# Performance work log

Measured on AMD Instinct MI355X. Metric: run time of the kernel, lower is better.

The kernel has to match this reference:

```python
import jax, jax.numpy as jnp
import numpy as np

B, N, IN_DIM, OUT_DIM, K = 64, 256, 512, 512, 8
DK = OUT_DIM // K  # per-kernel feature dim


def setup_inputs() -> dict:
    key = jax.random.key(0)
    k1, k2, k3, k4 = jax.random.split(key, 4)
    node_feats = jax.random.normal(k1, (B, N, IN_DIM), dtype=jnp.float32)
    adj = jax.random.uniform(k2, (B, K, N, N), dtype=jnp.float32)
    weight = jax.random.normal(k3, (IN_DIM, OUT_DIM), dtype=jnp.float32) * (1.0 / np.sqrt(IN_DIM))
    bias = jax.random.normal(k4, (OUT_DIM,), dtype=jnp.float32) * 0.01
    return {"node_feats": node_feats, "adj": adj, "weight": weight, "bias": bias}


def reference(node_feats, adj, weight, bias):
    # kernel linear + ReLU: (b, n, out_dim)
    h = jax.nn.relu(jnp.einsum('bni,io->bno', node_feats, weight) + bias)
    # split into kernel slots: (b, n, k, dk)
    h = h.reshape(B, N, K, DK)
    # graph.aggregate: per-kernel dense message passing over adjacency
    # out[b,n,k,d] = sum_m adj[b,k,n,m] * h[b,m,k,d]
    agg = jnp.einsum('bknm,bmkd->bnkd', adj, h)
    return agg.reshape(B, N, OUT_DIM)
```

## Files before the change

kernel.cpp:

```cpp
#include <hip/hip_runtime.h>
#include <hip/hip_bf16.h>


typedef __attribute__((ext_vector_type(8))) short short8;
typedef __attribute__((ext_vector_type(4))) float floatx4;

__device__ __forceinline__ unsigned short f2bf(float f) {
    union { float f; unsigned u; } v; v.f = f;
    unsigned r = v.u + 0x7FFFu + ((v.u >> 16) & 1u);
    return (unsigned short)(r >> 16);
}

__device__ __forceinline__ unsigned pk2bf(float a, float b) {
    union { __hip_bfloat162 h; unsigned u; } cv;
    cv.h = __float22bfloat162_rn(make_float2(a, b));
    return cv.u;
}

__global__ __launch_bounds__(256) void wt_kernel(const float* __restrict__ W,
                                                 unsigned short* __restrict__ Wt) {
    __shared__ unsigned short t_lds[64 * 66];
    const int tile = blockIdx.x;
    const int k0 = (tile >> 3) * 64;
    const int o0 = (tile & 7) * 64;
    const int t = threadIdx.x;
    const int c = t & 63;
    const int rb = t >> 6;
#pragma unroll
    for (int i = 0; i < 16; ++i) {
        int r = i * 4 + rb;
        t_lds[c * 66 + r] = f2bf(W[(size_t)(k0 + r) * 512 + o0 + c]);
    }
    __syncthreads();
#pragma unroll
    for (int i = 0; i < 16; ++i) {
        int o_r = i * 4 + rb;
        Wt[(size_t)(o0 + o_r) * 512 + k0 + c] = t_lds[o_r * 66 + c];
    }
}

__global__ __launch_bounds__(1024, 8) void fused_kernel(
    const float* __restrict__ X, const unsigned short* __restrict__ Wt,
    const float* __restrict__ bias, const float* __restrict__ adj,
    float* __restrict__ out) {
    __shared__ unsigned short ht[64 * 256];

    const int id = blockIdx.x;
    const int b = id & 63;
    const int ks = id >> 6;

    const int tid = threadIdx.x;
    const int lane = tid & 63, w = tid >> 6;
    const int lrow = lane & 15, quad = lane >> 4;

    const float* Xb = X + (size_t)b * 256 * 512;
    const unsigned short* Wslice = Wt + (size_t)ks * 64 * 512;

    floatx4 acc1[4];
    const floatx4 fzero = {0.f, 0.f, 0.f, 0.f};
#pragma unroll
    for (int j = 0; j < 4; ++j) acc1[j] = fzero;

    const float* xrow = Xb + (size_t)(w * 16 + lrow) * 512 + quad * 8;
    const unsigned short* wrow = Wslice + (size_t)lrow * 512 + quad * 8;

#pragma unroll 2
    for (int kb = 0; kb < 16; ++kb) {
        const int k0 = kb * 32;
        float4 xa = *(const float4*)(xrow + k0);
        float4 xc = *(const float4*)(xrow + k0 + 4);
        union { short8 s; unsigned u[4]; } af;
        af.u[0] = pk2bf(xa.x, xa.y);
        af.u[1] = pk2bf(xa.z, xa.w);
        af.u[2] = pk2bf(xc.x, xc.y);
        af.u[3] = pk2bf(xc.z, xc.w);
#pragma unroll
        for (int j = 0; j < 4; ++j) {
            short8 bfr = *(const short8*)(wrow + (size_t)j * 16 * 512 + k0);
            acc1[j] = __builtin_amdgcn_mfma_f32_16x16x32_bf16(af.s, bfr, acc1[j], 0, 0, 0);
        }
    }

#pragma unroll
    for (int j = 0; j < 4; ++j) {
        int d = 16 * j + lrow;
        float bv = bias[ks * 64 + d];
        floatx4 c = acc1[j];
        unsigned p01 = pk2bf(fmaxf(c.x + bv, 0.f), fmaxf(c.y + bv, 0.f));
        unsigned p23 = pk2bf(fmaxf(c.z + bv, 0.f), fmaxf(c.w + bv, 0.f));
        int jm = 2 * w + (quad >> 1);
        int phys = jm ^ (d & 7);
        unsigned* d32 = (unsigned*)(ht + d * 256 + phys * 8 + (quad & 1) * 4);
        d32[0] = p01; d32[1] = p23;
    }
    __syncthreads();

    const float* Abase = adj + ((size_t)(b * 8 + ks)) * 65536;
    const float* arow = Abase + (size_t)(w * 16 + lrow) * 256 + quad * 8;

    floatx4 acc[4];
#pragma unroll
    for (int j = 0; j < 4; ++j) acc[j] = fzero;

#pragma unroll 2
    for (int mt = 0; mt < 8; ++mt) {
        float4 a0 = *(const float4*)(arow + mt * 32);
        float4 a1 = *(const float4*)(arow + mt * 32 + 4);
        union { short8 s; unsigned u[4]; } afr;
        afr.u[0] = pk2bf(a0.x, a0.y);
        afr.u[1] = pk2bf(a0.z, a0.w);
        afr.u[2] = pk2bf(a1.x, a1.y);
        afr.u[3] = pk2bf(a1.z, a1.w);
        const int jm = 4 * mt + quad;
#pragma unroll
        for (int dt = 0; dt < 4; ++dt) {
            int d = dt * 16 + lrow;
            short8 bfr = *(const short8*)(ht + d * 256 + ((jm ^ (d & 7)) * 8));
            acc[dt] = __builtin_amdgcn_mfma_f32_16x16x32_bf16(afr.s, bfr, acc[dt], 0, 0, 0);
        }
    }

    const int n_g = w * 16 + quad * 4;
    float* dst = out + ((size_t)b * 256 + n_g) * 512 + ks * 64 + lrow;
#pragma unroll
    for (int dt = 0; dt < 4; ++dt) {
        float* p = dst + dt * 16;
        p[0 * 512] = acc[dt].x;
        p[1 * 512] = acc[dt].y;
        p[2 * 512] = acc[dt].z;
        p[3 * 512] = acc[dt].w;
    }
}

extern "C" void kernel_launch(void* const* d_in, const int* in_sizes, int n_in,
                              void* d_out, int out_size, void* d_ws, size_t ws_size,
                              hipStream_t stream) {
    const float* X    = (const float*)d_in[0];
    const float* adj  = (const float*)d_in[1];
    const float* W    = (const float*)d_in[2];
    const float* bias = (const float*)d_in[3];
    float* out = (float*)d_out;

    unsigned short* Wt = (unsigned short*)d_ws;

    wt_kernel<<<64, 256, 0, stream>>>(W, Wt);
    fused_kernel<<<512, 1024, 0, stream>>>(X, Wt, bias, adj, out);
}
```

Baseline: 305.6 us.

## Halve block size, give each wave two row tiles, and double-buffer global loads

The fused kernel now runs 512 threads per block instead of 1024, with each wave handling 32 rows (two 16-row tiles) in both GEMM stages. Each W/ht fragment load is then shared across two MFMA row groups. Both loops are fully unrolled and prefetch the next step's X/W and adj values into registers while the current step computes, and the first-stage adj load is issued before the LDS write. The goal is to hide global load latency and cut redundant B-fragment loads, at the cost of higher register pressure and fewer waves in flight per block.

```diff
diff --git a/kernel.cpp b/kernel.cpp
--- a/kernel.cpp
+++ b/kernel.cpp
@@ -39,7 +39,7 @@
     }
 }
 
-__global__ __launch_bounds__(1024, 8) void fused_kernel(
+__global__ __launch_bounds__(512, 4) void fused_kernel(
     const float* __restrict__ X, const unsigned short* __restrict__ Wt,
     const float* __restrict__ bias, const float* __restrict__ adj,
     float* __restrict__ out) {
@@ -52,83 +52,137 @@
     const int tid = threadIdx.x;
     const int lane = tid & 63, w = tid >> 6;
     const int lrow = lane & 15, quad = lane >> 4;
+    const int m0 = w * 32;
 
     const float* Xb = X + (size_t)b * 256 * 512;
     const unsigned short* Wslice = Wt + (size_t)ks * 64 * 512;
 
-    floatx4 acc1[4];
+    const float* xrow0 = Xb + (size_t)(m0 + lrow) * 512 + quad * 8;
+    const float* xrow1 = xrow0 + 16 * 512;
+    const unsigned short* wrow = Wslice + (size_t)lrow * 512 + quad * 8;
+
+    float bv[4];
+#pragma unroll
+    for (int j = 0; j < 4; ++j) bv[j] = bias[ks * 64 + 16 * j + lrow];
+
+    floatx4 acc1[2][4];
     const floatx4 fzero = {0.f, 0.f, 0.f, 0.f};
 #pragma unroll
-    for (int j = 0; j < 4; ++j) acc1[j] = fzero;
-
-    const float* xrow = Xb + (size_t)(w * 16 + lrow) * 512 + quad * 8;
-    const unsigned short* wrow = Wslice + (size_t)lrow * 512 + quad * 8;
-
-#pragma unroll 2
+    for (int g = 0; g < 2; ++g)
+#pragma unroll
+        for (int j = 0; j < 4; ++j) acc1[g][j] = fzero;
+
+    float4 xb_[2][2][2];
+    short8 wb_[2][4];
+
+#define LOAD_S1(buf, kb) do {                                           \
+        const int k0_ = (kb) * 32;                                      \
+        xb_[buf][0][0] = *(const float4*)(xrow0 + k0_);                 \
+        xb_[buf][0][1] = *(const float4*)(xrow0 + k0_ + 4);             \
+        xb_[buf][1][0] = *(const float4*)(xrow1 + k0_);                 \
+        xb_[buf][1][1] = *(const float4*)(xrow1 + k0_ + 4);             \
+        wb_[buf][0] = *(const short8*)(wrow + k0_);                     \
+        wb_[buf][1] = *(const short8*)(wrow + 16 * 512 + k0_);          \
+        wb_[buf][2] = *(const short8*)(wrow + 32 * 512 + k0_);          \
+        wb_[buf][3] = *(const short8*)(wrow + 48 * 512 + k0_);          \
+    } while (0)
+
+    LOAD_S1(0, 0);
+#pragma unroll
     for (int kb = 0; kb < 16; ++kb) {
-        const int k0 = kb * 32;
-        float4 xa = *(const float4*)(xrow + k0);
-        float4 xc = *(const float4*)(xrow + k0 + 4);
-        union { short8 s; unsigned u[4]; } af;
-        af.u[0] = pk2bf(xa.x, xa.y);
-        af.u[1] = pk2bf(xa.z, xa.w);
-        af.u[2] = pk2bf(xc.x, xc.y);
-        af.u[3] = pk2bf(xc.z, xc.w);
+        const int cur = kb & 1;
+        if (kb < 15) LOAD_S1(cur ^ 1, kb + 1);
+#pragma unroll
+        for (int g = 0; g < 2; ++g) {
+            union { short8 s; unsigned u[4]; } af;
+            const float4 va = xb_[cur][g][0], vc = xb_[cur][g][1];
+            af.u[0] = pk2bf(va.x, va.y);
+            af.u[1] = pk2bf(va.z, va.w);
+            af.u[2] = pk2bf(vc.x, vc.y);
+            af.u[3] = pk2bf(vc.z, vc.w);
+#pragma unroll
+            for (int j = 0; j < 4; ++j)
+                acc1[g][j] = __builtin_amdgcn_mfma_f32_16x16x32_bf16(
+                    af.s, wb_[cur][j], acc1[g][j], 0, 0, 0);
+        }
+    }
+#undef LOAD_S1
+
+    const float* Abase = adj + ((size_t)(b * 8 + ks)) * 65536;
+    const float* arow0 = Abase + (size_t)(m0 + lrow) * 256 + quad * 8;
+    const float* arow1 = arow0 + 16 * 256;
+
+    float4 ab_[2][2][2];
+#define LOAD_S2(buf, mt) do {                                           \
+        ab_[buf][0][0] = *(const float4*)(arow0 + (mt) * 32);           \
+        ab_[buf][0][1] = *(const float4*)(arow0 + (mt) * 32 + 4);       \
+        ab_[buf][1][0] = *(const float4*)(arow1 + (mt) * 32);           \
+        ab_[buf][1][1] = *(const float4*)(arow1 + (mt) * 32 + 4);       \
+    } while (0)
+
+    LOAD_S2(0, 0);
+
+#pragma unroll
+    for (int g = 0; g < 2; ++g) {
 #pragma unroll
         for (int j = 0; j < 4; ++j) {
-            short8 bfr = *(const short8*)(wrow + (size_t)j * 16 * 512 + k0);
-            acc1[j] = __builtin_amdgcn_mfma_f32_16x16x32_bf16(af.s, bfr, acc1[j], 0, 0, 0);
-        }
-    }
-
-#pragma unroll
-    for (int j = 0; j < 4; ++j) {
-        int d = 16 * j + lrow;
-        float bv = bias[ks * 64 + d];
-        floatx4 c = acc1[j];
-        unsigned p01 = pk2bf(fmaxf(c.x + bv, 0.f), fmaxf(c.y + bv, 0.f));
-        unsigned p23 = pk2bf(fmaxf(c.z + bv, 0.f), fmaxf(c.w + bv, 0.f));
-        int jm = 2 * w + (quad >> 1);
-        int phys = jm ^ (d & 7);
-        unsigned* d32 = (unsigned*)(ht + d * 256 + phys * 8 + (quad & 1) * 4);
-        d32[0] = p01; d32[1] = p23;
+            int d = 16 * j + lrow;
+            floatx4 c = acc1[g][j];
+            unsigned p01 = pk2bf(fmaxf(c.x + bv[j], 0.f), fmaxf(c.y + bv[j], 0.f));
+            unsigned p23 = pk2bf(fmaxf(c.z + bv[j], 0.f), fmaxf(c.w + bv[j], 0.f));
+            int jm = 4 * w + 2 * g + (quad >> 1);
+            int phys = jm ^ (d & 7);
+            unsigned* d32 = (unsigned*)(ht + d * 256 + phys * 8 + (quad & 1) * 4);
+            d32[0] = p01; d32[1] = p23;
+        }
     }
     __syncthreads();
 
-    const float* Abase = adj + ((size_t)(b * 8 + ks)) * 65536;
-    const float* arow = Abase + (size_t)(w * 16 + lrow) * 256 + quad * 8;
-
-    floatx4 acc[4];
-#pragma unroll
-    for (int j = 0; j < 4; ++j) acc[j] = fzero;
-
-#pragma unroll 2
+    floatx4 acc2[2][4];
+#pragma unroll
+    for (int g = 0; g < 2; ++g)
+#pragma unroll
+        for (int j = 0; j < 4; ++j) acc2[g][j] = fzero;
+
+#pragma unroll
     for (int mt = 0; mt < 8; ++mt) {
-        float4 a0 = *(const float4*)(arow + mt * 32);
-        float4 a1 = *(const float4*)(arow + mt * 32 + 4);
-        union { short8 s; unsigned u[4]; } afr;
-        afr.u[0] = pk2bf(a0.x, a0.y);
-        afr.u[1] = pk2bf(a0.z, a0.w);
-        afr.u[2] = pk2bf(a1.x, a1.y);
-        afr.u[3] = pk2bf(a1.z, a1.w);
+        const int cur = mt & 1;
+        if (mt < 7) LOAD_S2(cur ^ 1, mt + 1);
         const int jm = 4 * mt + quad;
+        short8 hfr[4];
 #pragma unroll
         for (int dt = 0; dt < 4; ++dt) {
             int d = dt * 16 + lrow;
-            short8 bfr = *(const short8*)(ht + d * 256 + ((jm ^ (d & 7)) * 8));
-            acc[dt] = __builtin_amdgcn_mfma_f32_16x16x32_bf16(afr.s, bfr, acc[dt], 0, 0, 0);
-        }
-    }
-
-    const int n_g = w * 16 + quad * 4;
-    float* dst = out + ((size_t)b * 256 + n_g) * 512 + ks * 64 + lrow;
-#pragma unroll
-    for (int dt = 0; dt < 4; ++dt) {
-        float* p = dst + dt * 16;
-        p[0 * 512] = acc[dt].x;
-        p[1 * 512] = acc[dt].y;
-        p[2 * 512] = acc[dt].z;
-        p[3 * 512] = acc[dt].w;
+            hfr[dt] = *(const short8*)(ht + d * 256 + ((jm ^ (d & 7)) * 8));
+        }
+#pragma unroll
+        for (int g = 0; g < 2; ++g) {
+            union { short8 s; unsigned u[4]; } af;
+            const float4 va = ab_[cur][g][0], vc = ab_[cur][g][1];
+            af.u[0] = pk2bf(va.x, va.y);
+            af.u[1] = pk2bf(va.z, va.w);
+            af.u[2] = pk2bf(vc.x, vc.y);
+            af.u[3] = pk2bf(vc.z, vc.w);
+#pragma unroll
+            for (int dt = 0; dt < 4; ++dt)
+                acc2[g][dt] = __builtin_amdgcn_mfma_f32_16x16x32_bf16(
+                    af.s, hfr[dt], acc2[g][dt], 0, 0, 0);
+        }
+    }
+#undef LOAD_S2
+
+#pragma unroll
+    for (int g = 0; g < 2; ++g) {
+        const int n_g = m0 + g * 16 + quad * 4;
+        float* dst = out + ((size_t)b * 256 + n_g) * 512 + ks * 64 + lrow;
+#pragma unroll
+        for (int dt = 0; dt < 4; ++dt) {
+            float* p = dst + dt * 16;
+            p[0 * 512] = acc2[g][dt].x;
+            p[1 * 512] = acc2[g][dt].y;
+            p[2 * 512] = acc2[g][dt].z;
+            p[3 * 512] = acc2[g][dt].w;
+        }
     }
 }
 
@@ -144,5 +198,5 @@
     unsigned short* Wt = (unsigned short*)d_ws;
 
     wt_kernel<<<64, 256, 0, stream>>>(W, Wt);
-    fused_kernel<<<512, 1024, 0, stream>>>(X, Wt, bias, adj, out);
-}
+    fused_kernel<<<512, 512, 0, stream>>>(X, Wt, bias, adj, out);
+}
```

Result: faster. 271.4 us (-11.2%).

## Split fused linear+aggregate kernel into two smaller-block kernels via global hT

Applied to the files above, without the earlier changes.

Replaces the single 512-block, 1024-thread fused kernel with a linear kernel and an aggregation kernel, each using 2048 blocks of 256 threads. The intermediate h is written transposed in bf16 to a workspace buffer in global memory instead of LDS. Blocks are remapped with an XCD-aware chunking so neighbouring work shares a die's L2. The goal is more blocks and better occupancy across CUs, at the cost of an extra global round trip for h, an extra launch, and X being reread per ks slice.

```diff
diff --git a/kernel.cpp b/kernel.cpp
--- a/kernel.cpp
+++ b/kernel.cpp
@@ -39,89 +39,109 @@
     }
 }
 
-__global__ __launch_bounds__(1024, 8) void fused_kernel(
+__device__ __forceinline__ int xcd_chunk(int bid) {
+    return (bid & 7) * 256 + (bid >> 3);
+}
+
+__global__ __launch_bounds__(256, 4) void lin_kernel(
     const float* __restrict__ X, const unsigned short* __restrict__ Wt,
-    const float* __restrict__ bias, const float* __restrict__ adj,
-    float* __restrict__ out) {
-    __shared__ unsigned short ht[64 * 256];
-
-    const int id = blockIdx.x;
-    const int b = id & 63;
-    const int ks = id >> 6;
+    const float* __restrict__ bias, unsigned short* __restrict__ hT) {
+    const int W_ = xcd_chunk(blockIdx.x);
+    const int ks = W_ & 7;
+    const int mt4 = (W_ >> 3) & 3;
+    const int b = W_ >> 5;
 
     const int tid = threadIdx.x;
     const int lane = tid & 63, w = tid >> 6;
     const int lrow = lane & 15, quad = lane >> 4;
 
-    const float* Xb = X + (size_t)b * 256 * 512;
-    const unsigned short* Wslice = Wt + (size_t)ks * 64 * 512;
+    const float* xp = X + (size_t)b * 131072
+                        + (size_t)(mt4 * 64 + w * 16 + lrow) * 512 + quad * 8;
+    const unsigned short* wp = Wt + (size_t)(ks * 64 + lrow) * 512 + quad * 8;
 
-    floatx4 acc1[4];
+    floatx4 acc[4];
     const floatx4 fzero = {0.f, 0.f, 0.f, 0.f};
 #pragma unroll
-    for (int j = 0; j < 4; ++j) acc1[j] = fzero;
-
-    const float* xrow = Xb + (size_t)(w * 16 + lrow) * 512 + quad * 8;
-    const unsigned short* wrow = Wslice + (size_t)lrow * 512 + quad * 8;
+    for (int j = 0; j < 4; ++j) acc[j] = fzero;
 
 #pragma unroll 2
     for (int kb = 0; kb < 16; ++kb) {
         const int k0 = kb * 32;
-        float4 xa = *(const float4*)(xrow + k0);
-        float4 xc = *(const float4*)(xrow + k0 + 4);
+        float4 x0 = *(const float4*)(xp + k0);
+        float4 x1 = *(const float4*)(xp + k0 + 4);
+        short8 wf0 = *(const short8*)(wp + k0);
+        short8 wf1 = *(const short8*)(wp + 8192 + k0);
+        short8 wf2 = *(const short8*)(wp + 16384 + k0);
+        short8 wf3 = *(const short8*)(wp + 24576 + k0);
         union { short8 s; unsigned u[4]; } af;
-        af.u[0] = pk2bf(xa.x, xa.y);
-        af.u[1] = pk2bf(xa.z, xa.w);
-        af.u[2] = pk2bf(xc.x, xc.y);
-        af.u[3] = pk2bf(xc.z, xc.w);
-#pragma unroll
-        for (int j = 0; j < 4; ++j) {
-            short8 bfr = *(const short8*)(wrow + (size_t)j * 16 * 512 + k0);
-            acc1[j] = __builtin_amdgcn_mfma_f32_16x16x32_bf16(af.s, bfr, acc1[j], 0, 0, 0);
-        }
+        af.u[0] = pk2bf(x0.x, x0.y);
+        af.u[1] = pk2bf(x0.z, x0.w);
+        af.u[2] = pk2bf(x1.x, x1.y);
+        af.u[3] = pk2bf(x1.z, x1.w);
+        acc[0] = __builtin_amdgcn_mfma_f32_16x16x32_bf16(af.s, wf0, acc[0], 0, 0, 0);
+        acc[1] = __builtin_amdgcn_mfma_f32_16x16x32_bf16(af.s, wf1, acc[1], 0, 0, 0);
+        acc[2] = __builtin_amdgcn_mfma_f32_16x16x32_bf16(af.s, wf2, acc[2], 0, 0, 0);
+        acc[3] = __builtin_amdgcn_mfma_f32_16x16x32_bf16(af.s, wf3, acc[3], 0, 0, 0);
     }
 
+    unsigned short* hslice = hT + ((size_t)(b * 8 + ks)) * 16384;
+    const int mg = mt4 * 64 + w * 16 + quad * 4;
 #pragma unroll
-    for (int j = 0; j < 4; ++j) {
-        int d = 16 * j + lrow;
-        float bv = bias[ks * 64 + d];
-        floatx4 c = acc1[j];
-        unsigned p01 = pk2bf(fmaxf(c.x + bv, 0.f), fmaxf(c.y + bv, 0.f));
-        unsigned p23 = pk2bf(fmaxf(c.z + bv, 0.f), fmaxf(c.w + bv, 0.f));
-        int jm = 2 * w + (quad >> 1);
-        int phys = jm ^ (d & 7);
-        unsigned* d32 = (unsigned*)(ht + d * 256 + phys * 8 + (quad & 1) * 4);
-        d32[0] = p01; d32[1] = p23;
+    for (int dt = 0; dt < 4; ++dt) {
+        const int d = dt * 16 + lrow;
+        const float bv = bias[ks * 64 + d];
+        floatx4 c = acc[dt];
+        uint2 pv;
+        pv.x = pk2bf(fmaxf(c.x + bv, 0.f), fmaxf(c.y + bv, 0.f));
+        pv.y = pk2bf(fmaxf(c.z + bv, 0.f), fmaxf(c.w + bv, 0.f));
+        *(uint2*)(hslice + d * 256 + mg) = pv;
     }
-    __syncthreads();
+}
 
-    const float* Abase = adj + ((size_t)(b * 8 + ks)) * 65536;
-    const float* arow = Abase + (size_t)(w * 16 + lrow) * 256 + quad * 8;
+__global__ __launch_bounds__(256, 4) void agg_kernel(
+    const unsigned short* __restrict__ hT, const float* __restrict__ adj,
+    float* __restrict__ out) {
+    const int W_ = xcd_chunk(blockIdx.x);
+    const int nt = W_ & 3;
+    const int ks = (W_ >> 2) & 7;
+    const int b = W_ >> 5;
+
+    const int tid = threadIdx.x;
+    const int lane = tid & 63, w = tid >> 6;
+    const int lrow = lane & 15, quad = lane >> 4;
+
+    const float* ap = adj + ((size_t)(b * 8 + ks)) * 65536
+                          + (size_t)(nt * 64 + w * 16 + lrow) * 256 + quad * 8;
+    const unsigned short* hp = hT + ((size_t)(b * 8 + ks)) * 16384
+                                  + lrow * 256 + quad * 8;
 
     floatx4 acc[4];
+    const floatx4 fzero = {0.f, 0.f, 0.f, 0.f};
 #pragma unroll
     for (int j = 0; j < 4; ++j) acc[j] = fzero;
 
 #pragma unroll 2
     for (int mt = 0; mt < 8; ++mt) {
-        float4 a0 = *(const float4*)(arow + mt * 32);
-        float4 a1 = *(const float4*)(arow + mt * 32 + 4);
-        union { short8 s; unsigned u[4]; } afr;
-        afr.u[0] = pk2bf(a0.x, a0.y);
-        afr.u[1] = pk2bf(a0.z, a0.w);
-        afr.u[2] = pk2bf(a1.x, a1.y);
-        afr.u[3] = pk2bf(a1.z, a1.w);
-        const int jm = 4 * mt + quad;
-#pragma unroll
-        for (int dt = 0; dt < 4; ++dt) {
-            int d = dt * 16 + lrow;
-            short8 bfr = *(const short8*)(ht + d * 256 + ((jm ^ (d & 7)) * 8));
-            acc[dt] = __builtin_amdgcn_mfma_f32_16x16x32_bf16(afr.s, bfr, acc[dt], 0, 0, 0);
-        }
+        const int m0 = mt * 32;
+        float4 a0 = *(const float4*)(ap + m0);
+        float4 a1 = *(const float4*)(ap + m0 + 4);
+        short8 h0 = *(const short8*)(hp + m0);
+        short8 h1 = *(const short8*)(hp + 4096 + m0);
+        short8 h2 = *(const short8*)(hp + 8192 + m0);
+        short8 h3 = *(const short8*)(hp + 12288 + m0);
+        union { short8 s; unsigned u[4]; } af;
+        af.u[0] = pk2bf(a0.x, a0.y);
+        af.u[1] = pk2bf(a0.z, a0.w);
+        af.u[2] = pk2bf(a1.x, a1.y);
+        af.u[3] = pk2bf(a1.z, a1.w);
+        acc[0] = __builtin_amdgcn_mfma_f32_16x16x32_bf16(af.s, h0, acc[0], 0, 0, 0);
+        acc[1] = __builtin_amdgcn_mfma_f32_16x16x32_bf16(af.s, h1, acc[1], 0, 0, 0);
+        acc[2] = __builtin_amdgcn_mfma_f32_16x16x32_bf16(af.s, h2, acc[2], 0, 0, 0);
+        acc[3] = __builtin_amdgcn_mfma_f32_16x16x32_bf16(af.s, h3, acc[3], 0, 0, 0);
     }
 
-    const int n_g = w * 16 + quad * 4;
-    float* dst = out + ((size_t)b * 256 + n_g) * 512 + ks * 64 + lrow;
+    const int n0 = nt * 64 + w * 16 + quad * 4;
+    float* dst = out + ((size_t)b * 256 + n0) * 512 + ks * 64 + lrow;
 #pragma unroll
     for (int dt = 0; dt < 4; ++dt) {
         float* p = dst + dt * 16;
@@ -142,7 +162,9 @@
     float* out = (float*)d_out;
 
     unsigned short* Wt = (unsigned short*)d_ws;
+    unsigned short* hT = Wt + 512 * 512;
 
     wt_kernel<<<64, 256, 0, stream>>>(W, Wt);
-    fused_kernel<<<512, 1024, 0, stream>>>(X, Wt, bias, adj, out);
+    lin_kernel<<<2048, 256, 0, stream>>>(X, Wt, bias, hT);
+    agg_kernel<<<2048, 256, 0, stream>>>(hT, adj, out);
 }
```

Measured after the change: 318.0 us. +4.1%, slower.

## Split fused kernel into linear and aggregation kernels with double-buffered LDS staging

Applied to the files above, without the earlier changes.

Replaces the single fused linear+aggregate kernel with three kernels: a W fragment-layout prep kernel, a linear kernel that writes a bf16 intermediate h to workspace in MFMA-fragment order, and an aggregation kernel. Both main kernels use 256-thread blocks, double-buffered LDS staging of the fp32-to-bf16 converted inputs, a 2x4 MFMA tile per wave, and a blockIdx swizzle. The aim is higher occupancy and overlap of global loads with MFMA work. In exchange it adds a workspace round-trip for h and an extra launch.

```diff
diff --git a/kernel.cpp b/kernel.cpp
--- a/kernel.cpp
+++ b/kernel.cpp
@@ -17,118 +17,196 @@
     return cv.u;
 }
 
-__global__ __launch_bounds__(256) void wt_kernel(const float* __restrict__ W,
-                                                 unsigned short* __restrict__ Wt) {
-    __shared__ unsigned short t_lds[64 * 66];
-    const int tile = blockIdx.x;
-    const int k0 = (tile >> 3) * 64;
-    const int o0 = (tile & 7) * 64;
-    const int t = threadIdx.x;
-    const int c = t & 63;
-    const int rb = t >> 6;
-#pragma unroll
-    for (int i = 0; i < 16; ++i) {
-        int r = i * 4 + rb;
-        t_lds[c * 66 + r] = f2bf(W[(size_t)(k0 + r) * 512 + o0 + c]);
+__global__ __launch_bounds__(256) void wfrag_kernel(const float* __restrict__ W,
+                                                    unsigned short* __restrict__ Wf) {
+    __shared__ unsigned short t[32 * 66];
+    const int blk = blockIdx.x;
+    const int k0 = (blk & 15) * 32;
+    const int o0 = (blk >> 4) * 64;
+    const int tid = threadIdx.x;
+#pragma unroll
+    for (int j = 0; j < 8; ++j) {
+        int idx = tid + j * 256;
+        int oc = idx & 63, kr = idx >> 6;
+        t[kr * 66 + oc] = f2bf(W[(size_t)(k0 + kr) * 512 + o0 + oc]);
     }
     __syncthreads();
 #pragma unroll
-    for (int i = 0; i < 16; ++i) {
-        int o_r = i * 4 + rb;
-        Wt[(size_t)(o0 + o_r) * 512 + k0 + c] = t_lds[o_r * 66 + c];
-    }
-}
-
-__global__ __launch_bounds__(1024, 8) void fused_kernel(
-    const float* __restrict__ X, const unsigned short* __restrict__ Wt,
-    const float* __restrict__ bias, const float* __restrict__ adj,
-    float* __restrict__ out) {
-    __shared__ unsigned short ht[64 * 256];
-
-    const int id = blockIdx.x;
-    const int b = id & 63;
-    const int ks = id >> 6;
+    for (int j = 0; j < 8; ++j) {
+        int idx = tid + j * 256;
+        int kk = idx & 31, dr = idx >> 5;
+        Wf[(size_t)blk * 2048 + dr * 32 + kk] = t[kk * 66 + dr];
+    }
+}
+
+__global__ __launch_bounds__(256, 5) void lin_kernel(
+    const float* __restrict__ X, const unsigned short* __restrict__ Wf,
+    const float* __restrict__ bias, unsigned short* __restrict__ hF) {
+    __shared__ unsigned short xt[2][128 * 40];
+
+    const int W_ = (blockIdx.x & 7) * 128 + (blockIdx.x >> 3);
+    const int mh = W_ & 1;
+    const int ks = (W_ >> 1) & 7;
+    const int b  = W_ >> 4;
 
     const int tid = threadIdx.x;
     const int lane = tid & 63, w = tid >> 6;
     const int lrow = lane & 15, quad = lane >> 4;
 
-    const float* Xb = X + (size_t)b * 256 * 512;
-    const unsigned short* Wslice = Wt + (size_t)ks * 64 * 512;
-
-    floatx4 acc1[4];
+    const float* xsrc = X + (size_t)b * 131072
+                          + (size_t)(mh * 128 + (tid >> 1)) * 512 + (tid & 1) * 16;
+    const int xw = (tid >> 1) * 40 + (tid & 1) * 16;
+
+    const unsigned short* wfp = Wf + (size_t)ks * 32768 + lrow * 32 + quad * 8;
+
+    float bv[4];
+#pragma unroll
+    for (int dt = 0; dt < 4; ++dt) bv[dt] = bias[ks * 64 + dt * 16 + lrow];
+
+    floatx4 acc[2][4];
     const floatx4 fzero = {0.f, 0.f, 0.f, 0.f};
 #pragma unroll
-    for (int j = 0; j < 4; ++j) acc1[j] = fzero;
-
-    const float* xrow = Xb + (size_t)(w * 16 + lrow) * 512 + quad * 8;
-    const unsigned short* wrow = Wslice + (size_t)lrow * 512 + quad * 8;
-
-#pragma unroll 2
+    for (int g = 0; g < 2; ++g)
+#pragma unroll
+        for (int j = 0; j < 4; ++j) acc[g][j] = fzero;
+
+    float4 r[4];
+#define LLOAD(kb) do {                                                  \
+        r[0] = *(const float4*)(xsrc + (kb) * 32);                      \
+        r[1] = *(const float4*)(xsrc + (kb) * 32 + 4);                  \
+        r[2] = *(const float4*)(xsrc + (kb) * 32 + 8);                  \
+        r[3] = *(const float4*)(xsrc + (kb) * 32 + 12);                 \
+    } while (0)
+#define LWRITE(buf) do {                                                \
+        union { short8 s; unsigned u[4]; } t0_, t1_;                    \
+        t0_.u[0] = pk2bf(r[0].x, r[0].y); t0_.u[1] = pk2bf(r[0].z, r[0].w); \
+        t0_.u[2] = pk2bf(r[1].x, r[1].y); t0_.u[3] = pk2bf(r[1].z, r[1].w); \
+        t1_.u[0] = pk2bf(r[2].x, r[2].y); t1_.u[1] = pk2bf(r[2].z, r[2].w); \
+        t1_.u[2] = pk2bf(r[3].x, r[3].y); t1_.u[3] = pk2bf(r[3].z, r[3].w); \
+        *(short8*)(xt[buf] + xw) = t0_.s;                               \
+        *(short8*)(xt[buf] + xw + 8) = t1_.s;                           \
+    } while (0)
+
+    LLOAD(0);
+    LWRITE(0);
+    LLOAD(1);
+    __syncthreads();
+
+#pragma unroll
     for (int kb = 0; kb < 16; ++kb) {
-        const int k0 = kb * 32;
-        float4 xa = *(const float4*)(xrow + k0);
-        float4 xc = *(const float4*)(xrow + k0 + 4);
-        union { short8 s; unsigned u[4]; } af;
-        af.u[0] = pk2bf(xa.x, xa.y);
-        af.u[1] = pk2bf(xa.z, xa.w);
-        af.u[2] = pk2bf(xc.x, xc.y);
-        af.u[3] = pk2bf(xc.z, xc.w);
-#pragma unroll
-        for (int j = 0; j < 4; ++j) {
-            short8 bfr = *(const short8*)(wrow + (size_t)j * 16 * 512 + k0);
-            acc1[j] = __builtin_amdgcn_mfma_f32_16x16x32_bf16(af.s, bfr, acc1[j], 0, 0, 0);
-        }
-    }
-
-#pragma unroll
-    for (int j = 0; j < 4; ++j) {
-        int d = 16 * j + lrow;
-        float bv = bias[ks * 64 + d];
-        floatx4 c = acc1[j];
-        unsigned p01 = pk2bf(fmaxf(c.x + bv, 0.f), fmaxf(c.y + bv, 0.f));
-        unsigned p23 = pk2bf(fmaxf(c.z + bv, 0.f), fmaxf(c.w + bv, 0.f));
-        int jm = 2 * w + (quad >> 1);
-        int phys = jm ^ (d & 7);
-        unsigned* d32 = (unsigned*)(ht + d * 256 + phys * 8 + (quad & 1) * 4);
-        d32[0] = p01; d32[1] = p23;
-    }
+        const int buf = kb & 1;
+        if (kb < 15) {
+            LWRITE(buf ^ 1);
+            if (kb < 14) LLOAD(kb + 2);
+        }
+        short8 a0 = *(const short8*)(xt[buf] + (w * 32 + lrow) * 40 + quad * 8);
+        short8 a1 = *(const short8*)(xt[buf] + (w * 32 + 16 + lrow) * 40 + quad * 8);
+#pragma unroll
+        for (int dt = 0; dt < 4; ++dt) {
+            short8 wfr = *(const short8*)(wfp + kb * 2048 + dt * 512);
+            acc[0][dt] = __builtin_amdgcn_mfma_f32_16x16x32_bf16(a0, wfr, acc[0][dt], 0, 0, 0);
+            acc[1][dt] = __builtin_amdgcn_mfma_f32_16x16x32_bf16(a1, wfr, acc[1][dt], 0, 0, 0);
+        }
+        if (kb < 15) __syncthreads();
+    }
+#undef LLOAD
+#undef LWRITE
+
+    unsigned short* hs = hF + (size_t)(b * 8 + ks) * 16384 + (size_t)(mh * 4 + w) * 2048;
+#pragma unroll
+    for (int g = 0; g < 2; ++g) {
+#pragma unroll
+        for (int dt = 0; dt < 4; ++dt) {
+            floatx4 c = acc[g][dt];
+            uint2 pv;
+            pv.x = pk2bf(fmaxf(c.x + bv[dt], 0.f), fmaxf(c.y + bv[dt], 0.f));
+            pv.y = pk2bf(fmaxf(c.z + bv[dt], 0.f), fmaxf(c.w + bv[dt], 0.f));
+            *(uint2*)(hs + dt * 512 + lrow * 32 + g * 16 + quad * 4) = pv;
+        }
+    }
+}
+
+__global__ __launch_bounds__(256, 5) void agg_kernel(
+    const unsigned short* __restrict__ hF, const float* __restrict__ adj,
+    float* __restrict__ out) {
+    __shared__ unsigned short at[2][128 * 40];
+
+    const int W_ = (blockIdx.x & 7) * 128 + (blockIdx.x >> 3);
+    const int nt = W_ & 1;
+    const int ks = (W_ >> 1) & 7;
+    const int b  = W_ >> 4;
+
+    const int tid = threadIdx.x;
+    const int lane = tid & 63, w = tid >> 6;
+    const int lrow = lane & 15, quad = lane >> 4;
+
+    const float* asrc = adj + (size_t)(b * 8 + ks) * 65536
+                            + (size_t)(nt * 128 + (tid >> 1)) * 256 + (tid & 1) * 16;
+    const int aw = (tid >> 1) * 40 + (tid & 1) * 16;
+
+    const unsigned short* hfp = hF + (size_t)(b * 8 + ks) * 16384 + lrow * 32 + quad * 8;
+
+    floatx4 acc[2][4];
+    const floatx4 fzero = {0.f, 0.f, 0.f, 0.f};
+#pragma unroll
+    for (int g = 0; g < 2; ++g)
+#pragma unroll
+        for (int j = 0; j < 4; ++j) acc[g][j] = fzero;
+
+    float4 r[4];
+#define ALOAD(mt) do {                                                  \
+        r[0] = *(const float4*)(asrc + (mt) * 32);                      \
+        r[1] = *(const float4*)(asrc + (mt) * 32 + 4);                  \
+        r[2] = *(const float4*)(asrc + (mt) * 32 + 8);                  \
+        r[3] = *(const float4*)(asrc + (mt) * 32 + 12);                 \
+    } while (0)
+#define AWRITE(buf) do {                                                \
+        union { short8 s; unsigned u[4]; } t0_, t1_;                    \
+        t0_.u[0] = pk2bf(r[0].x, r[0].y); t0_.u[1] = pk2bf(r[0].z, r[0].w); \
+        t0_.u[2] = pk2bf(r[1].x, r[1].y); t0_.u[3] = pk2bf(r[1].z, r[1].w); \
+        t1_.u[0] = pk2bf(r[2].x, r[2].y); t1_.u[1] = pk2bf(r[2].z, r[2].w); \
+        t1_.u[2] = pk2bf(r[3].x, r[3].y); t1_.u[3] = pk2bf(r[3].z, r[3].w); \
+        *(short8*)(at[buf] + aw) = t0_.s;                               \
+        *(short8*)(at[buf] + aw + 8) = t1_.s;                           \
+    } while (0)
+
+    ALOAD(0);
+    AWRITE(0);
+    ALOAD(1);
     __syncthreads();
 
-    const float* Abase = adj + ((size_t)(b * 8 + ks)) * 65536;
-    const float* arow = Abase + (size_t)(w * 16 + lrow) * 256 + quad * 8;
-
-    floatx4 acc[4];
-#pragma unroll
-    for (int j = 0; j < 4; ++j) acc[j] = fzero;
-
-#pragma unroll 2
+#pragma unroll
     for (int mt = 0; mt < 8; ++mt) {
-        float4 a0 = *(const float4*)(arow + mt * 32);
-        float4 a1 = *(const float4*)(arow + mt * 32 + 4);
-        union { short8 s; unsigned u[4]; } afr;
-        afr.u[0] = pk2bf(a0.x, a0.y);
-        afr.u[1] = pk2bf(a0.z, a0.w);
-        afr.u[2] = pk2bf(a1.x, a1.y);
-        afr.u[3] = pk2bf(a1.z, a1.w);
-        const int jm = 4 * mt + quad;
-#pragma unroll
-        for (int dt = 0; dt < 4; ++dt) {
-            int d = dt * 16 + lrow;
-            short8 bfr = *(const short8*)(ht + d * 256 + ((jm ^ (d & 7)) * 8));
-            acc[dt] = __builtin_amdgcn_mfma_f32_16x16x32_bf16(afr.s, bfr, acc[dt], 0, 0, 0);
-        }
-    }
-
-    const int n_g = w * 16 + quad * 4;
-    float* dst = out + ((size_t)b * 256 + n_g) * 512 + ks * 64 + lrow;
-#pragma unroll
-    for (int dt = 0; dt < 4; ++dt) {
-        float* p = dst + dt * 16;
-        p[0 * 512] = acc[dt].x;
-        p[1 * 512] = acc[dt].y;
-        p[2 * 512] = acc[dt].z;
-        p[3 * 512] = acc[dt].w;
+        const int buf = mt & 1;
+        if (mt < 7) {
+            AWRITE(buf ^ 1);
+            if (mt < 6) ALOAD(mt + 2);
+        }
+        short8 a0 = *(const short8*)(at[buf] + (w * 32 + lrow) * 40 + quad * 8);
+        short8 a1 = *(const short8*)(at[buf] + (w * 32 + 16 + lrow) * 40 + quad * 8);
+#pragma unroll
+        for (int dt = 0; dt < 4; ++dt) {
+            short8 hfr = *(const short8*)(hfp + mt * 2048 + dt * 512);
+            acc[0][dt] = __builtin_amdgcn_mfma_f32_16x16x32_bf16(a0, hfr, acc[0][dt], 0, 0, 0);
+            acc[1][dt] = __builtin_amdgcn_mfma_f32_16x16x32_bf16(a1, hfr, acc[1][dt], 0, 0, 0);
+        }
+        if (mt < 7) __syncthreads();
+    }
+#undef ALOAD
+#undef AWRITE
+
+#pragma unroll
+    for (int g = 0; g < 2; ++g) {
+        const int n0 = nt * 128 + w * 32 + g * 16 + quad * 4;
+        float* dst = out + ((size_t)b * 256 + n0) * 512 + ks * 64 + lrow;
+#pragma unroll
+        for (int dt = 0; dt < 4; ++dt) {
+            float* p = dst + dt * 16;
+            p[0 * 512] = acc[g][dt].x;
+            p[1 * 512] = acc[g][dt].y;
+            p[2 * 512] = acc[g][dt].z;
+            p[3 * 512] = acc[g][dt].w;
+        }
     }
 }
 
@@ -141,8 +219,10 @@
     const float* bias = (const float*)d_in[3];
     float* out = (float*)d_out;
 
-    unsigned short* Wt = (unsigned short*)d_ws;
-
-    wt_kernel<<<64, 256, 0, stream>>>(W, Wt);
-    fused_kernel<<<512, 1024, 0, stream>>>(X, Wt, bias, adj, out);
-}
+    unsigned short* Wf = (unsigned short*)d_ws;
+    unsigned short* hF = Wf + 512 * 512;
+
+    wfrag_kernel<<<128, 256, 0, stream>>>(W, Wf);
+    lin_kernel<<<1024, 256, 0, stream>>>(X, Wf, bias, hF);
+    agg_kernel<<<1024, 256, 0, stream>>>(hF, adj, out);
+}
```

Result: faster. 271.5 us (-11.2%).
